# Kernel optimization log

Measured on AMD Instinct MI355X. Metric: run time of the kernel, lower is better.

Reference implementation:

```python
import jax, jax.numpy as jnp
import numpy as np

N_NODES = 50000
N_EDGES = 800000
FEAT_DIM = 64
NUM_RELS = 8


def setup_inputs() -> dict:
    key = jax.random.key(0)
    k1, k2, k3, k4, k5 = jax.random.split(key, 5)
    features = jax.random.normal(k1, (N_NODES, FEAT_DIM), dtype=jnp.float32)
    # xavier_uniform with relu gain ~= sqrt(2)*sqrt(6/(D+D))
    limit = np.sqrt(2.0) * np.sqrt(6.0 / (FEAT_DIM + FEAT_DIM))
    weight_r = jax.random.uniform(k2, (NUM_RELS, FEAT_DIM, FEAT_DIM), dtype=jnp.float32,
                                  minval=-limit, maxval=limit)
    src = jax.random.randint(k3, (N_EDGES,), 0, N_NODES, dtype=jnp.int64 if jax.config.jax_enable_x64 else jnp.int32)
    dst = jax.random.randint(k4, (N_EDGES,), 0, N_NODES, dtype=src.dtype)
    etype = jax.random.randint(k5, (N_EDGES,), 0, NUM_RELS, dtype=src.dtype)
    return {"features": features, "weight_r": weight_r, "src": src, "dst": dst, "etype": etype}


def reference(features, weight_r, src, dst, etype):
    N, D = features.shape
    c = 0.2
    # in-degree of each destination node (DGL 'deg' node data)
    deg = jax.ops.segment_sum(jnp.ones(dst.shape, dtype=features.dtype), dst, num_segments=N)
    # relation-batched matmul: h @ W_r for every relation, then gather per edge.
    # [R, N, D] = 8*50000*64 floats -- cheap vs. materializing [E, D, D] weights.
    hw = jnp.einsum('nd,rdf->rnf', features, weight_r)
    msg = hw[etype, src] / deg[dst][:, None]          # [E, D]
    M = jax.ops.segment_sum(msg, dst, num_segments=N)  # scatter-sum mailbox reduce
    updated = jax.nn.relu(c * features + (1.0 - c) * M)
    # DGL only applies reduce to nodes that received messages; others keep h.
    return jnp.where((deg > 0)[:, None], updated, features)
```

## Files before the change

### kernel.cpp

```cpp
#include <hip/hip_runtime.h>
#include <hip/hip_bf16.h>

#define N_NODES 50000
#define N_EDGES 800000
#define FEAT 64
#define NRELS 8
#define NSUP 196
#define SCAP 5120
#define NBP 196
#define FB_BLOCKS 782
#define NPB 32
#define NBUCK 1563
#define BCAP 768

typedef __attribute__((ext_vector_type(8))) short bf16x8;
typedef __attribute__((ext_vector_type(4))) float f32x4;

static __host__ __device__ inline size_t align256(size_t x) { return (x + 255) & ~(size_t)255; }

__device__ inline unsigned short f2b(float f) {
    unsigned u = __builtin_bit_cast(unsigned, f);
    unsigned r = (u + 0x7fffu + ((u >> 16) & 1u)) >> 16;
    return (unsigned short)r;
}
__device__ inline float b2f(unsigned short u) {
    unsigned v = ((unsigned)u) << 16;
    return __builtin_bit_cast(float, v);
}

__global__ void bfill_kernel(const int* __restrict__ dst, const int* __restrict__ srcv,
                             const int* __restrict__ et, const float* __restrict__ W,
                             const float* __restrict__ feat,
                             int* __restrict__ bcnt, int* __restrict__ tmp,
                             unsigned short* __restrict__ WtT,
                             unsigned short* __restrict__ Fb, int E, int N) {
    const int t = threadIdx.x;

    if (blockIdx.x >= NBP) {
        const int fbb = blockIdx.x - NBP;
        if (fbb < 32) {
            int i4 = fbb * 256 + t;
            float4 v = ((const float4*)W)[i4];
            int bse = i4 * 4;
            int f0 = bse & 63;
            int rd = bse >> 6;
            int d  = rd & 63;
            int r  = rd >> 6;
            unsigned short* w0 = WtT + ((size_t)(r * 64 + f0) * 64 + d);
            w0[0 * 64] = f2b(v.x);
            w0[1 * 64] = f2b(v.y);
            w0[2 * 64] = f2b(v.z);
            w0[3 * 64] = f2b(v.w);
        }
        const int node = fbb * 64 + (t >> 2);
        if (node >= N) return;
        const int seg = t & 3;
        const float4* F4 = (const float4*)feat + (size_t)node * 16 + seg * 4;
        float4 v0 = F4[0], v1 = F4[1], v2 = F4[2], v3 = F4[3];
        bf16x8 b0, b1;
        b0[0] = (short)f2b(v0.x); b0[1] = (short)f2b(v0.y);
        b0[2] = (short)f2b(v0.z); b0[3] = (short)f2b(v0.w);
        b0[4] = (short)f2b(v1.x); b0[5] = (short)f2b(v1.y);
        b0[6] = (short)f2b(v1.z); b0[7] = (short)f2b(v1.w);
        b1[0] = (short)f2b(v2.x); b1[1] = (short)f2b(v2.y);
        b1[2] = (short)f2b(v2.z); b1[3] = (short)f2b(v2.w);
        b1[4] = (short)f2b(v3.x); b1[5] = (short)f2b(v3.y);
        b1[6] = (short)f2b(v3.z); b1[7] = (short)f2b(v3.w);
        *(bf16x8*)(Fb + (size_t)node * 64 + seg * 16)     = b0;
        *(bf16x8*)(Fb + (size_t)node * 64 + seg * 16 + 8) = b1;
        return;
    }

    __shared__ int pkL[4096];
    __shared__ unsigned char supL[4096];
    __shared__ int hist[NSUP];
    __shared__ int lbase[NSUP];
    __shared__ int gbase[NSUP];
    __shared__ int lcur[NSUP];
    __shared__ int wsum[4];
    __shared__ int totS;

    for (int j = t; j < NSUP; j += 256) hist[j] = 0;
    __syncthreads();

    const int4* dst4 = (const int4*)dst;
    const int4* src4 = (const int4*)srcv;
    const int4* et4  = (const int4*)et;
    const int n4 = E >> 2;
    int sup[16], pk[16];
#pragma unroll
    for (int k = 0; k < 4; k++) {
        int i4 = blockIdx.x * 1024 + t + k * 256;
        if (i4 < n4) {
            int4 d = dst4[i4];
            int4 s = src4[i4];
            int4 r = et4[i4];
            const int dd[4] = {d.x, d.y, d.z, d.w};
            const int ss[4] = {s.x, s.y, s.z, s.w};
            const int rr[4] = {r.x, r.y, r.z, r.w};
#pragma unroll
            for (int j = 0; j < 4; j++) {
                int idx = k * 4 + j;
                sup[idx] = dd[j] >> 8;
                pk[idx] = (ss[j] & 0xFFFF) | (rr[j] << 16) | ((dd[j] & 255) << 19);
                atomicAdd(&hist[sup[idx]], 1);
            }
        } else {
#pragma unroll
            for (int j = 0; j < 4; j++) sup[k * 4 + j] = -1;
        }
    }
    __syncthreads();

    const int myc = (t < NSUP) ? hist[t] : 0;
    int x = myc;
#pragma unroll
    for (int o = 1; o < 64; o <<= 1) {
        int u_ = __shfl_up(x, o);
        if ((t & 63) >= o) x += u_;
    }
    if ((t & 63) == 63) wsum[t >> 6] = x;
    __syncthreads();
    {
        int add = 0;
        const int wv = t >> 6;
        if (wv > 0) add += wsum[0];
        if (wv > 1) add += wsum[1];
        if (wv > 2) add += wsum[2];
        x += add;
    }
    const int ex = x - myc;
    if (t < NSUP) {
        lbase[t] = ex;
        lcur[t] = ex;
        gbase[t] = t * SCAP + ((myc > 0) ? atomicAdd(&bcnt[t], myc) : 0);
    }
    if (t == 255) totS = x;
    __syncthreads();

#pragma unroll
    for (int k = 0; k < 16; k++) {
        if (sup[k] >= 0) {
            int p = atomicAdd(&lcur[sup[k]], 1);
            pkL[p] = pk[k];
            supL[p] = (unsigned char)sup[k];
        }
    }
    __syncthreads();

    const int total = totS;
    for (int s0 = t; s0 < total; s0 += 256) {
        int sp = supL[s0];
        int pos = gbase[sp] + (s0 - lbase[sp]);
        if (pos < (sp + 1) * SCAP)
            tmp[pos] = pkL[s0];
    }
}

__global__ __launch_bounds__(256, 4) void fuse_kernel(
    const int* __restrict__ bcnt, const int* __restrict__ tmp,
    const unsigned short* __restrict__ Fb,
    const unsigned short* __restrict__ WtT, const float* __restrict__ feat,
    float* __restrict__ out, int N) {
    __shared__ unsigned short Sb[NRELS][NPB][64];
    __shared__ int sedge[BCAP];
    __shared__ int hist[256];
    __shared__ int noff[NPB + 1];
    __shared__ int wsum[4];
    const int t = threadIdx.x;
    const int bkt = blockIdx.x;
    const int n0 = bkt * NPB;
    const int nn = min(NPB, N - n0);
    const int gid = t >> 3, q = t & 7;
    const int sup = bkt >> 3, sub = bkt & 7;

    {
        f32x4 z = {0.f, 0.f, 0.f, 0.f};
        f32x4* zp = (f32x4*)&Sb[0][0][0];
#pragma unroll
        for (int i = 0; i < 8; i++) zp[t + 256 * i] = z;
    }
    hist[t] = 0;
    __syncthreads();

    const int cnt = min(bcnt[sup], SCAP);
    const int* tb = tmp + (size_t)sup * SCAP;
    for (int i = t; i < cnt; i += 256) {
        int v = tb[i];
        if (((v >> 24) & 7) == sub)
            atomicAdd(&hist[(((v >> 19) & 31) << 3) | ((v >> 16) & 7)], 1);
    }
    __syncthreads();
    const int myc = hist[t];
    int x = myc;
#pragma unroll
    for (int o = 1; o < 64; o <<= 1) {
        int u_ = __shfl_up(x, o);
        if ((t & 63) >= o) x += u_;
    }
    if ((t & 63) == 63) wsum[t >> 6] = x;
    __syncthreads();
    {
        int add = 0;
        const int wv = t >> 6;
        if (wv > 0) add += wsum[0];
        if (wv > 1) add += wsum[1];
        if (wv > 2) add += wsum[2];
        x += add;
    }
    const int ex = x - myc;
    if ((t & 7) == 0) noff[t >> 3] = ex;
    if (t == 255) noff[NPB] = ex + myc;
    hist[t] = ex;
    __syncthreads();
    for (int i = t; i < cnt; i += 256) {
        int v = tb[i];
        if (((v >> 24) & 7) == sub) {
            int p = atomicAdd(&hist[(((v >> 19) & 31) << 3) | ((v >> 16) & 7)], 1);
            if (p < BCAP)
                sedge[p] = v;
        }
    }
    __syncthreads();

    int b = 0, e = 0;
    if (gid < nn) {
        b = min(noff[gid], BCAP);
        e = min(noff[gid + 1], BCAP);
    }
    if (gid < nn && b < e) {
        const int swz = (q ^ (gid & 7)) * 8;
        unsigned short* srow = &Sb[0][0][0] + (size_t)gid * 64 + swz;
        float a[8] = {0.f, 0.f, 0.f, 0.f, 0.f, 0.f, 0.f, 0.f};
        int curR = -1;

        auto flushS = [&](int rel) {
            bf16x8 v;
#pragma unroll
            for (int k = 0; k < 8; k++) v[k] = (short)f2b(a[k]);
            *(bf16x8*)(srow + (size_t)rel * (NPB * 64)) = v;
        };
        auto issue = [&](int cb, int (&pk)[4], bf16x8 (&u)[4]) {
#pragma unroll
            for (int j = 0; j < 4; j++) {
                int p = (cb + j < e) ? sedge[cb + j] : -1;
                pk[j] = p;
                if (p >= 0)
                    u[j] = *(const bf16x8*)(Fb + (size_t)(p & 0xFFFF) * 64 + q * 8);
            }
        };
        auto consume = [&](int (&pk)[4], bf16x8 (&u)[4]) {
#pragma unroll
            for (int j = 0; j < 4; j++) {
                int p = pk[j];
                if (p >= 0) {
                    bf16x8 uu = u[j];
                    int rel = (p >> 16) & 7;
                    if (rel != curR) {
                        if (curR >= 0) flushS(curR);
                        curR = rel;
#pragma unroll
                        for (int k = 0; k < 8; k++) a[k] = b2f((unsigned short)uu[k]);
                    } else {
#pragma unroll
                        for (int k = 0; k < 8; k++) a[k] += b2f((unsigned short)uu[k]);
                    }
                }
            }
        };

        bf16x8 z8 = {0, 0, 0, 0, 0, 0, 0, 0};
        int pkA[4] = {-1, -1, -1, -1}, pkB[4] = {-1, -1, -1, -1};
        bf16x8 uA[4] = {z8, z8, z8, z8}, uB[4] = {z8, z8, z8, z8};

        issue(b, pkA, uA);
        __builtin_amdgcn_sched_barrier(0);
#pragma unroll
        for (int c = 0; c < 8; c++) {
            const int nb = b + (c + 1) * 4;
            if ((c & 1) == 0) {
                if (c < 7 && nb < e) issue(nb, pkB, uB);
                __builtin_amdgcn_sched_barrier(0);
                consume(pkA, uA);
            } else {
                if (c < 7 && nb < e) issue(nb, pkA, uA);
                __builtin_amdgcn_sched_barrier(0);
                consume(pkB, uB);
            }
            if (nb >= e) break;
        }
        for (int i = b + 32; i < e; i++) {
            int p = sedge[i];
            bf16x8 uu = *(const bf16x8*)(Fb + (size_t)(p & 0xFFFF) * 64 + q * 8);
            int rel = (p >> 16) & 7;
            if (rel != curR) {
                if (curR >= 0) flushS(curR);
                curR = rel;
#pragma unroll
                for (int k = 0; k < 8; k++) a[k] = b2f((unsigned short)uu[k]);
            } else {
#pragma unroll
                for (int k = 0; k < 8; k++) a[k] += b2f((unsigned short)uu[k]);
            }
        }
        if (curR >= 0) flushS(curR);
    }

    float4 h0e = make_float4(0.f, 0.f, 0.f, 0.f), h1e = h0e;
    const int ef0 = q * 8;
    if (gid < nn) {
        const float4* fp = (const float4*)feat + (size_t)(n0 + gid) * 16 + (ef0 >> 2);
        h0e = fp[0];
        h1e = fp[1];
    }
    __syncthreads();

    const int w = t >> 6, l = t & 63, col = l & 15, quad = l >> 4;
    f32x4 acc0 = {0.f, 0.f, 0.f, 0.f}, acc1 = {0.f, 0.f, 0.f, 0.f};
    const int sw0 = (quad ^ (col & 7)) * 8;
    const int sw1 = ((quad + 4) ^ (col & 7)) * 8;
#pragma unroll
    for (int r = 0; r < NRELS; r++) {
        const unsigned short* wp = WtT + (size_t)r * 4096 + ((w * 16 + col) * 64 + quad * 8);
        bf16x8 b0 = *(const bf16x8*)wp;
        bf16x8 b1 = *(const bf16x8*)(wp + 32);
        const unsigned short* Sr = &Sb[0][0][0] + (size_t)r * (NPB * 64);
        bf16x8 a0 = *(const bf16x8*)&Sr[col * 64 + sw0];
        bf16x8 a1 = *(const bf16x8*)&Sr[col * 64 + sw1];
        bf16x8 c0 = *(const bf16x8*)&Sr[(16 + col) * 64 + sw0];
        bf16x8 c1 = *(const bf16x8*)&Sr[(16 + col) * 64 + sw1];
        acc0 = __builtin_amdgcn_mfma_f32_16x16x32_bf16(a0, b0, acc0, 0, 0, 0);
        acc0 = __builtin_amdgcn_mfma_f32_16x16x32_bf16(a1, b1, acc0, 0, 0, 0);
        acc1 = __builtin_amdgcn_mfma_f32_16x16x32_bf16(c0, b0, acc1, 0, 0, 0);
        acc1 = __builtin_amdgcn_mfma_f32_16x16x32_bf16(c1, b1, acc1, 0, 0, 0);
    }
    __syncthreads();

    float* C = (float*)&Sb[0][0][0];
#pragma unroll
    for (int i = 0; i < 4; i++) {
        C[(quad * 4 + i) * 72 + w * 16 + col]        = acc0[i];
        C[(16 + quad * 4 + i) * 72 + w * 16 + col]   = acc1[i];
    }
    __syncthreads();

    if (gid < nn) {
        const int gn = n0 + gid;
        const int deg = e - b;
        float4 m0 = *(const float4*)&C[gid * 72 + ef0];
        float4 m1 = *(const float4*)&C[gid * 72 + ef0 + 4];
        float4 r0, r1;
        if (deg > 0) {
            float inv = 0.8f / (float)deg;
            r0.x = fmaxf(0.2f * h0e.x + m0.x * inv, 0.f);
            r0.y = fmaxf(0.2f * h0e.y + m0.y * inv, 0.f);
            r0.z = fmaxf(0.2f * h0e.z + m0.z * inv, 0.f);
            r0.w = fmaxf(0.2f * h0e.w + m0.w * inv, 0.f);
            r1.x = fmaxf(0.2f * h1e.x + m1.x * inv, 0.f);
            r1.y = fmaxf(0.2f * h1e.y + m1.y * inv, 0.f);
            r1.z = fmaxf(0.2f * h1e.z + m1.z * inv, 0.f);
            r1.w = fmaxf(0.2f * h1e.w + m1.w * inv, 0.f);
        } else {
            r0 = h0e; r1 = h1e;
        }
        float4* op = (float4*)out + (size_t)gn * 16 + (ef0 >> 2);
        op[0] = r0;
        op[1] = r1;
    }
}

__global__ void degf_kernel(const int* __restrict__ dst, float* __restrict__ deg, int E) {
    int e = blockIdx.x * blockDim.x + threadIdx.x;
    if (e < E) atomicAdd(deg + dst[e], 1.0f);
}

__global__ void otf_kernel(const int* __restrict__ src, const int* __restrict__ dst,
                           const int* __restrict__ et, const float* __restrict__ feat,
                           const float* __restrict__ W, float* __restrict__ out, int E) {
    int wid = (blockIdx.x * blockDim.x + threadIdx.x) >> 6;
    int l = threadIdx.x & 63;
    if (wid >= E) return;
    int s = src[wid], dd = dst[wid], r = et[wid];
    float fv = feat[(size_t)s * 64 + l];
    const float* Wr = W + (size_t)r * 4096;
    float acc = 0.f;
#pragma unroll
    for (int d = 0; d < 64; d++) {
        float a = __shfl(fv, d);
        acc += a * Wr[d * 64 + l];
    }
    atomicAdd(out + (size_t)dd * 64 + l, acc);
}

__global__ void final_kernel(const float* __restrict__ feat, const float* __restrict__ deg,
                             float* __restrict__ out, int N) {
    int i = blockIdx.x * blockDim.x + threadIdx.x;
    if (i >= N * 16) return;
    int n = i >> 4;
    float d = deg[n];
    float4 f = ((const float4*)feat)[i];
    float4 m = ((float4*)out)[i];
    float4 res;
    if (d > 0.f) {
        float inv = 0.8f / d;
        res.x = fmaxf(0.2f * f.x + m.x * inv, 0.f);
        res.y = fmaxf(0.2f * f.y + m.y * inv, 0.f);
        res.z = fmaxf(0.2f * f.z + m.z * inv, 0.f);
        res.w = fmaxf(0.2f * f.w + m.w * inv, 0.f);
    } else {
        res = f;
    }
    ((float4*)out)[i] = res;
}

extern "C" void kernel_launch(void* const* d_in, const int* in_sizes, int n_in,
                              void* d_out, int out_size, void* d_ws, size_t ws_size,
                              hipStream_t stream) {
    const float* feat = (const float*)d_in[0];
    const float* W    = (const float*)d_in[1];
    const int*   src  = (const int*)d_in[2];
    const int*   dst  = (const int*)d_in[3];
    const int*   et   = (const int*)d_in[4];
    float* out = (float*)d_out;

    const int N = N_NODES, E = N_EDGES;

    char* p = (char*)d_ws;
    int* bcnt  = (int*)p;  p += align256((size_t)NSUP * 4);
    int* tmp   = (int*)p;  p += align256((size_t)NSUP * SCAP * 4);
    unsigned short* WtT = (unsigned short*)p;
    p += align256((size_t)NRELS * FEAT * FEAT * 2);
    unsigned short* Fb = (unsigned short*)p;
    p += align256((size_t)N * FEAT * 2);
    size_t need_full = (size_t)(p - (char*)d_ws);

    if (ws_size >= need_full) {
        hipMemsetAsync(bcnt, 0, (size_t)NSUP * 4, stream);
        bfill_kernel<<<NBP + FB_BLOCKS, 256, 0, stream>>>(dst, src, et, W, feat,
                                                          bcnt, tmp, WtT, Fb, E, N);
        fuse_kernel<<<NBUCK, 256, 0, stream>>>(bcnt, tmp, Fb, WtT, feat, out, N);
    } else {
        float* deg = (float*)d_ws;
        hipMemsetAsync(out, 0, (size_t)N * FEAT * 4, stream);
        hipMemsetAsync(deg, 0, (size_t)N * 4, stream);
        degf_kernel<<<(E + 255) / 256, 256, 0, stream>>>(dst, deg, E);
        otf_kernel<<<(E + 3) / 4, 256, 0, stream>>>(src, dst, et, feat, W, out, E);
        final_kernel<<<(N * 16 + 255) / 256, 256, 0, stream>>>(feat, deg, out, N);
    }
}
```

Measured before the change: 140.2 us.

## Replace atomic bucket scatter with deterministic per-block segments plus dedicated sort kernel

The bucketing pass no longer takes global atomics on per-supernode counters. Each block writes its locally sorted edge segment and a per-supernode count/offset table. A new sort kernel, one 1024-thread block per supernode, gathers these runs, counting-sorts them by (node, relation) and emits per-node CSR offsets. The fuse kernel then only loads its contiguous edge slice instead of rescanning the whole supernode buffer twice with histograms. The cost is an extra kernel launch and an extra global round trip of the edge list.

Result: faster. 128.6 us (-8.3%).

```diff
diff --git a/kernel.cpp b/kernel.cpp
--- a/kernel.cpp
+++ b/kernel.cpp
@@ -31,7 +31,7 @@
 __global__ void bfill_kernel(const int* __restrict__ dst, const int* __restrict__ srcv,
                              const int* __restrict__ et, const float* __restrict__ W,
                              const float* __restrict__ feat,
-                             int* __restrict__ bcnt, int* __restrict__ tmp,
+                             int* __restrict__ tmp, int* __restrict__ cnts,
                              unsigned short* __restrict__ WtT,
                              unsigned short* __restrict__ Fb, int E, int N) {
     const int t = threadIdx.x;
@@ -72,13 +72,12 @@
     }
 
     __shared__ int pkL[4096];
-    __shared__ unsigned char supL[4096];
     __shared__ int hist[NSUP];
     __shared__ int lbase[NSUP];
-    __shared__ int gbase[NSUP];
     __shared__ int lcur[NSUP];
     __shared__ int wsum[4];
     __shared__ int totS;
+    const int blk = blockIdx.x;
 
     for (int j = t; j < NSUP; j += 256) hist[j] = 0;
     __syncthreads();
@@ -90,7 +89,7 @@
     int sup[16], pk[16];
 #pragma unroll
     for (int k = 0; k < 4; k++) {
-        int i4 = blockIdx.x * 1024 + t + k * 256;
+        int i4 = blk * 1024 + t + k * 256;
         if (i4 < n4) {
             int4 d = dst4[i4];
             int4 s = src4[i4];
@@ -133,7 +132,7 @@
     if (t < NSUP) {
         lbase[t] = ex;
         lcur[t] = ex;
-        gbase[t] = t * SCAP + ((myc > 0) ? atomicAdd(&bcnt[t], myc) : 0);
+        cnts[t * NBP + blk] = (ex << 16) | myc;
     }
     if (t == 255) totS = x;
     __syncthreads();
@@ -143,90 +142,154 @@
         if (sup[k] >= 0) {
             int p = atomicAdd(&lcur[sup[k]], 1);
             pkL[p] = pk[k];
-            supL[p] = (unsigned char)sup[k];
         }
     }
     __syncthreads();
 
     const int total = totS;
-    for (int s0 = t; s0 < total; s0 += 256) {
-        int sp = supL[s0];
-        int pos = gbase[sp] + (s0 - lbase[sp]);
-        if (pos < (sp + 1) * SCAP)
-            tmp[pos] = pkL[s0];
-    }
-}
-
-__global__ __launch_bounds__(256, 4) void fuse_kernel(
-    const int* __restrict__ bcnt, const int* __restrict__ tmp,
-    const unsigned short* __restrict__ Fb,
-    const unsigned short* __restrict__ WtT, const float* __restrict__ feat,
-    float* __restrict__ out, int N) {
-    __shared__ unsigned short Sb[NRELS][NPB][64];
-    __shared__ int sedge[BCAP];
-    __shared__ int hist[256];
-    __shared__ int noff[NPB + 1];
-    __shared__ int wsum[4];
+    int* seg = tmp + (size_t)blk * 4096;
+    for (int i = t; i < total; i += 256) seg[i] = pkL[i];
+}
+
+__global__ __launch_bounds__(1024, 1) void sortk_kernel(
+    const int* __restrict__ tmp, const int* __restrict__ cnts,
+    int* __restrict__ spk, int* __restrict__ off_s, int* __restrict__ off_e,
+    int N) {
+    __shared__ int pkL[SCAP];
+    __shared__ int sorted_[SCAP];
+    __shared__ int hist2[2048];
+    __shared__ int runB[NBP];
+    __shared__ int runS[NBP];
+    __shared__ int runC[NBP];
+    __shared__ int wsum[16];
+    __shared__ int totEs;
     const int t = threadIdx.x;
-    const int bkt = blockIdx.x;
-    const int n0 = bkt * NPB;
-    const int nn = min(NPB, N - n0);
-    const int gid = t >> 3, q = t & 7;
-    const int sup = bkt >> 3, sub = bkt & 7;
-
-    {
-        f32x4 z = {0.f, 0.f, 0.f, 0.f};
-        f32x4* zp = (f32x4*)&Sb[0][0][0];
-#pragma unroll
-        for (int i = 0; i < 8; i++) zp[t + 256 * i] = z;
-    }
-    hist[t] = 0;
-    __syncthreads();
-
-    const int cnt = min(bcnt[sup], SCAP);
-    const int* tb = tmp + (size_t)sup * SCAP;
-    for (int i = t; i < cnt; i += 256) {
-        int v = tb[i];
-        if (((v >> 24) & 7) == sub)
-            atomicAdd(&hist[(((v >> 19) & 31) << 3) | ((v >> 16) & 7)], 1);
-    }
-    __syncthreads();
-    const int myc = hist[t];
-    int x = myc;
-#pragma unroll
-    for (int o = 1; o < 64; o <<= 1) {
-        int u_ = __shfl_up(x, o);
-        if ((t & 63) >= o) x += u_;
-    }
-    if ((t & 63) == 63) wsum[t >> 6] = x;
-    __syncthreads();
-    {
+    const int s = blockIdx.x;
+
+    if (t < NBP) {
+        int pc = cnts[s * NBP + t];
+        runS[t] = pc >> 16;
+        runC[t] = pc & 0xFFFF;
+    }
+    __syncthreads();
+    if (t < 256) {
+        const int myc = (t < NBP) ? runC[t] : 0;
+        int x = myc;
+#pragma unroll
+        for (int o = 1; o < 64; o <<= 1) {
+            int u_ = __shfl_up(x, o);
+            if ((t & 63) >= o) x += u_;
+        }
+        if ((t & 63) == 63) wsum[t >> 6] = x;
+        __syncthreads();
         int add = 0;
         const int wv = t >> 6;
         if (wv > 0) add += wsum[0];
         if (wv > 1) add += wsum[1];
         if (wv > 2) add += wsum[2];
         x += add;
-    }
-    const int ex = x - myc;
-    if ((t & 7) == 0) noff[t >> 3] = ex;
-    if (t == 255) noff[NPB] = ex + myc;
-    hist[t] = ex;
-    __syncthreads();
-    for (int i = t; i < cnt; i += 256) {
-        int v = tb[i];
-        if (((v >> 24) & 7) == sub) {
-            int p = atomicAdd(&hist[(((v >> 19) & 31) << 3) | ((v >> 16) & 7)], 1);
-            if (p < BCAP)
-                sedge[p] = v;
-        }
-    }
-    __syncthreads();
-
-    int b = 0, e = 0;
+        if (t < NBP) runB[t] = x - myc;
+        if (t == 255) totEs = min(x, SCAP);
+    } else {
+        __syncthreads();
+    }
+    __syncthreads();
+    const int totE = totEs;
+
+    {
+        const int w = t >> 6, lane = t & 63;
+        for (int r = w; r < NBP; r += 16) {
+            const int c = runC[r];
+            const int bse = runB[r];
+            const int* srcp = tmp + (size_t)r * 4096 + runS[r];
+            for (int i = lane; i < c; i += 64) {
+                int o = bse + i;
+                if (o < SCAP) pkL[o] = srcp[i];
+            }
+        }
+    }
+    hist2[t] = 0;
+    hist2[t + 1024] = 0;
+    __syncthreads();
+
+    for (int i = t; i < totE; i += 1024) {
+        int v = pkL[i];
+        atomicAdd(&hist2[(((v >> 19) & 255) << 3) | ((v >> 16) & 7)], 1);
+    }
+    __syncthreads();
+    const int loc0 = hist2[2 * t], loc1 = hist2[2 * t + 1];
+    {
+        const int T = loc0 + loc1;
+        int x = T;
+#pragma unroll
+        for (int o = 1; o < 64; o <<= 1) {
+            int u_ = __shfl_up(x, o);
+            if ((t & 63) >= o) x += u_;
+        }
+        if ((t & 63) == 63) wsum[t >> 6] = x;
+        __syncthreads();
+        int add = 0;
+        const int wv = t >> 6;
+#pragma unroll
+        for (int v_ = 0; v_ < 16; v_++) if (v_ < wv) add += wsum[v_];
+        x += add;
+        hist2[2 * t]     = x - T;
+        hist2[2 * t + 1] = x - T + loc0;
+    }
+    __syncthreads();
+    if (t < 256) {
+        const int gn = s * 256 + t;
+        if (gn < N) {
+            const int st = hist2[8 * t];
+            const int en = (t == 255) ? totE : hist2[8 * t + 8];
+            off_s[gn] = s * SCAP + st;
+            off_e[gn] = s * SCAP + en;
+        }
+    }
+    __syncthreads();
+    for (int i = t; i < totE; i += 1024) {
+        int v = pkL[i];
+        int pos = atomicAdd(&hist2[(((v >> 19) & 255) << 3) | ((v >> 16) & 7)], 1);
+        if (pos < SCAP) sorted_[pos] = v;
+    }
+    __syncthreads();
+    for (int i = t; i < totE; i += 1024) spk[(size_t)s * SCAP + i] = sorted_[i];
+}
+
+__global__ __launch_bounds__(256, 4) void fuse_kernel(
+    const int* __restrict__ spk, const int* __restrict__ off_s,
+    const int* __restrict__ off_e, const unsigned short* __restrict__ Fb,
+    const unsigned short* __restrict__ WtT, const float* __restrict__ feat,
+    float* __restrict__ out, int N) {
+    __shared__ unsigned short Sb[NRELS][NPB][64];
+    __shared__ int sedge[BCAP];
+    const int t = threadIdx.x;
+    const int bkt = blockIdx.x;
+    const int n0 = bkt * NPB;
+    const int nn = min(NPB, N - n0);
+    const int gid = t >> 3, q = t & 7;
+
+    {
+        f32x4 z = {0.f, 0.f, 0.f, 0.f};
+        f32x4* zp = (f32x4*)&Sb[0][0][0];
+#pragma unroll
+        for (int i = 0; i < 8; i++) zp[t + 256 * i] = z;
+    }
+
+    const int b0 = off_s[n0];
+    const int eL = off_e[n0 + nn - 1];
+    for (int i = b0 + t; i < eL; i += 256) {
+        int o = i - b0;
+        if (o < BCAP) sedge[o] = spk[i];
+    }
+    __syncthreads();
+
+    int b = 0, e = 0, deg = 0;
     if (gid < nn) {
-        b = min(noff[gid], BCAP);
-        e = min(noff[gid + 1], BCAP);
+        const int rb = off_s[n0 + gid], re = off_e[n0 + gid];
+        deg = re - rb;
+        b = rb - b0;
+        e = min(re - b0, BCAP);
     }
     if (gid < nn && b < e) {
         const int swz = (q ^ (gid & 7)) * 8;
@@ -346,7 +409,6 @@
 
     if (gid < nn) {
         const int gn = n0 + gid;
-        const int deg = e - b;
         float4 m0 = *(const float4*)&C[gid * 72 + ef0];
         float4 m1 = *(const float4*)&C[gid * 72 + ef0 + 4];
         float4 r0, r1;
@@ -426,8 +488,11 @@
     const int N = N_NODES, E = N_EDGES;
 
     char* p = (char*)d_ws;
-    int* bcnt  = (int*)p;  p += align256((size_t)NSUP * 4);
-    int* tmp   = (int*)p;  p += align256((size_t)NSUP * SCAP * 4);
+    int* tmp   = (int*)p;  p += align256((size_t)NBP * 4096 * 4);
+    int* cnts  = (int*)p;  p += align256((size_t)NSUP * NBP * 4);
+    int* spk   = (int*)p;  p += align256((size_t)NSUP * SCAP * 4);
+    int* off_s = (int*)p;  p += align256((size_t)N * 4);
+    int* off_e = (int*)p;  p += align256((size_t)N * 4);
     unsigned short* WtT = (unsigned short*)p;
     p += align256((size_t)NRELS * FEAT * FEAT * 2);
     unsigned short* Fb = (unsigned short*)p;
@@ -435,10 +500,11 @@
     size_t need_full = (size_t)(p - (char*)d_ws);
 
     if (ws_size >= need_full) {
-        hipMemsetAsync(bcnt, 0, (size_t)NSUP * 4, stream);
         bfill_kernel<<<NBP + FB_BLOCKS, 256, 0, stream>>>(dst, src, et, W, feat,
-                                                          bcnt, tmp, WtT, Fb, E, N);
-        fuse_kernel<<<NBUCK, 256, 0, stream>>>(bcnt, tmp, Fb, WtT, feat, out, N);
+                                                          tmp, cnts, WtT, Fb, E, N);
+        sortk_kernel<<<NSUP, 1024, 0, stream>>>(tmp, cnts, spk, off_s, off_e, N);
+        fuse_kernel<<<NBUCK, 256, 0, stream>>>(spk, off_s, off_e, Fb, WtT,
+                                               feat, out, N);
     } else {
         float* deg = (float*)d_ws;
         hipMemsetAsync(out, 0, (size_t)N * FEAT * 4, stream);
```
